# Performance work log

Hardware: AMD Instinct MI355X
Metric: run time of the kernel (lower is better)

Reference implementation:

```python
import jax, jax.numpy as jnp
from jax import lax
import numpy as np

N, T, D_OBS, D_Z, D_U = 32, 1024, 128, 64, 8
H_ENC, H_BW, H_DYN = 256, 128, 256
D_A = 2 * D_Z  # natural-parameter dim (mean-part, precision-part)


def setup_inputs() -> dict:
    key = jax.random.key(0)
    ks = jax.random.split(key, 16)

    def w(k, shape):
        return (jax.random.normal(k, shape, jnp.float32) / np.sqrt(shape[0]).astype(np.float32))

    return {
        "t": jnp.broadcast_to(jnp.arange(T, dtype=jnp.int32), (N, T)),
        "y": jax.random.normal(ks[0], (N, T, D_OBS), jnp.float32),
        "u": 0.1 * jax.random.normal(ks[1], (N, T, D_U), jnp.float32),
        "enc_w1": w(ks[2], (D_OBS, H_ENC)),
        "enc_b1": jnp.zeros((H_ENC,), jnp.float32),
        "enc_w2": w(ks[3], (H_ENC, D_A)),
        "enc_b2": jnp.zeros((D_A,), jnp.float32),
        "bw_wa": w(ks[4], (D_A, H_BW)),
        "bw_wh": w(ks[5], (H_BW, H_BW)),
        "bw_b": jnp.zeros((H_BW,), jnp.float32),
        "bw_wo": w(ks[6], (H_BW, D_A)),
        "bw_bo": jnp.zeros((D_A,), jnp.float32),
        "dyn_w1": w(ks[7], (D_Z + D_U, H_DYN)),
        "dyn_b1": jnp.zeros((H_DYN,), jnp.float32),
        "dyn_w2": w(ks[8], (H_DYN, D_Z)),
        "dyn_b2": jnp.zeros((D_Z,), jnp.float32),
        "q_raw": 0.1 * jax.random.normal(ks[9], (D_Z,), jnp.float32),
        "m0": jnp.zeros((D_Z,), jnp.float32),
        "v0": jnp.ones((D_Z,), jnp.float32),
    }


def _constrain_natural(nat):
    # DiagMVN: first half is the mean-natural-param, second half must be <= 0
    e1, e2 = nat[..., :D_Z], nat[..., D_Z:]
    return jnp.concatenate([e1, -jax.nn.softplus(e2)], axis=-1)


def reference(t, y, u, enc_w1, enc_b1, enc_w2, enc_b2,
              bw_wa, bw_wh, bw_b, bw_wo, bw_bo,
              dyn_w1, dyn_b1, dyn_w2, dyn_b2, q_raw, m0, v0):
    # --- local obs encoder (per-step MLP), dropout prob = 0.0 so mask == 1 ---
    h = jnp.tanh(jnp.einsum('ntd,dh->nth', y, enc_w1) + enc_b1)
    a = jnp.einsum('nth,ha->nta', h, enc_w2) + enc_b2          # [N,T,2Dz]

    # --- backward encoder: reverse recurrence over time (pseudo mode) ---
    a_t = jnp.swapaxes(a, 0, 1)                                # [T,N,2Dz]

    def bw_step(h_next, a_step):
        hcell = jnp.tanh(a_step @ bw_wa + h_next @ bw_wh + bw_b)
        return hcell, hcell @ bw_wo + bw_bo

    _, b_t = lax.scan(bw_step, jnp.zeros((N, H_BW), a.dtype), a_t, reverse=True)
    alpha = _constrain_natural(b_t)                            # [T,N,2Dz]

    # --- vmap'd sequential natural-parameter filter over time ---
    Q = jax.nn.softplus(q_raw)                                 # diag state noise
    u_t = jnp.swapaxes(u, 0, 1)                                # [T,N,Du]

    def step(carry, xs):
        m, v = carry
        alpha_step, u_step = xs
        x = jnp.concatenate([m, u_step], axis=-1)
        m_p = jnp.tanh(x @ dyn_w1 + dyn_b1) @ dyn_w2 + dyn_b2  # predictive mean
        v_p = v + Q                                            # predictive var
        e1 = m_p / v_p + alpha_step[..., :D_Z]
        e2 = -0.5 / v_p + alpha_step[..., D_Z:]                # stays < 0
        v_s = -0.5 / e2
        m_s = v_s * e1
        return (m_s, v_s), (jnp.concatenate([m_s, v_s], -1),
                            jnp.concatenate([m_p, v_p], -1))

    m_init = jnp.broadcast_to(m0, (N, D_Z))
    v_init = jnp.broadcast_to(v0, (N, D_Z))
    _, (moment_s, moment_p) = lax.scan(step, (m_init, v_init), (alpha, u_t))

    out = jnp.concatenate([moment_s, moment_p], axis=-1)       # [T,N,4Dz]
    return jnp.swapaxes(out, 0, 1)                             # [N,T,4Dz]
```

## Files before the change

kernel.cpp:

```cpp
#include <hip/hip_runtime.h>
#include <math.h>

#define T_LEN 1024
#define NB 32

typedef _Float16 h2 __attribute__((ext_vector_type(2)));

__device__ __forceinline__ h2 f2h2(float f) { return __builtin_bit_cast(h2, f); }

__device__ __forceinline__ float dot2(h2 a, h2 b, float c) {
#if __has_builtin(__builtin_amdgcn_fdot2)
    return __builtin_amdgcn_fdot2(a, b, c, false);
#else
    return fmaf((float)a[0], (float)b[0], fmaf((float)a[1], (float)b[1], c));
#endif
}

#define DPP_ADD(v, ctrl) do { \
    int _xi = __builtin_bit_cast(int, v); \
    int _yi = __builtin_amdgcn_update_dpp(_xi, _xi, (ctrl), 0xF, 0xF, true); \
    v += __builtin_bit_cast(float, _yi); } while (0)

__device__ __forceinline__ float softplus_f(float x) {
    return fmaxf(x, 0.f) + log1pf(expf(-fabsf(x)));
}

__device__ __forceinline__ float fast_tanh(float x) {
    float e = __builtin_amdgcn_exp2f(x * 2.88539008177792681472f);
    float r = __builtin_amdgcn_rcpf(1.f + e);
    return 1.f - 2.f * r;
}

__device__ __forceinline__ void bar_sync() {
    asm volatile("s_waitcnt lgkmcnt(0)" ::: "memory");
    __builtin_amdgcn_s_barrier();
    asm volatile("" ::: "memory");
}

__global__ __launch_bounds__(256) void k_encoder(
    const float* __restrict__ y, const float* __restrict__ u,
    const float* __restrict__ w1, const float* __restrict__ b1,
    const float* __restrict__ w2, const float* __restrict__ b2,
    const float* __restrict__ wa, const float* __restrict__ bb,
    const float* __restrict__ dynw1, const float* __restrict__ dynb1,
    float* __restrict__ apre, float* __restrict__ preU)
{
    __shared__ float ly[8][128];
    __shared__ float lh[8][256];
    __shared__ float la[8][128];
    __shared__ float lu[8][8];
    const int tid = threadIdx.x;
    const int row0 = blockIdx.x * 8;

    ((float4*)&ly[0][0])[tid] = ((const float4*)(y + (size_t)row0 * 128))[tid];
    if (tid < 16)
        ((float4*)&lu[0][0])[tid] = ((const float4*)(u + (size_t)row0 * 8))[tid];
    __syncthreads();

    {
        float acc[8] = {0,0,0,0,0,0,0,0};
        for (int i = 0; i < 128; i += 4) {
            float w0 = w1[(i+0)*256 + tid];
            float w1v = w1[(i+1)*256 + tid];
            float w2v = w1[(i+2)*256 + tid];
            float w3 = w1[(i+3)*256 + tid];
            #pragma unroll
            for (int r = 0; r < 8; ++r) {
                float4 yv = *(const float4*)&ly[r][i];
                acc[r] += yv.x*w0 + yv.y*w1v + yv.z*w2v + yv.w*w3;
            }
        }
        float bias = b1[tid];
        #pragma unroll
        for (int r = 0; r < 8; ++r) lh[r][tid] = fast_tanh(acc[r] + bias);
    }
    __syncthreads();

    {
        const int d = tid & 127, rh = tid >> 7;
        float acc[4] = {0,0,0,0};
        for (int i = 0; i < 256; i += 4) {
            float w0 = w2[(i+0)*128 + d];
            float w1v = w2[(i+1)*128 + d];
            float w2v = w2[(i+2)*128 + d];
            float w3 = w2[(i+3)*128 + d];
            #pragma unroll
            for (int q = 0; q < 4; ++q) {
                float4 hv = *(const float4*)&lh[rh*4+q][i];
                acc[q] += hv.x*w0 + hv.y*w1v + hv.z*w2v + hv.w*w3;
            }
        }
        float bias = b2[d];
        #pragma unroll
        for (int q = 0; q < 4; ++q) la[rh*4+q][d] = acc[q] + bias;
    }
    __syncthreads();

    {
        const int j = tid & 127, rh = tid >> 7;
        float acc[4] = {0,0,0,0};
        for (int i = 0; i < 128; i += 4) {
            float w0 = wa[(i+0)*128 + j];
            float w1v = wa[(i+1)*128 + j];
            float w2v = wa[(i+2)*128 + j];
            float w3 = wa[(i+3)*128 + j];
            #pragma unroll
            for (int q = 0; q < 4; ++q) {
                float4 av = *(const float4*)&la[rh*4+q][i];
                acc[q] += av.x*w0 + av.y*w1v + av.z*w2v + av.w*w3;
            }
        }
        float bias = bb[j];
        #pragma unroll
        for (int q = 0; q < 4; ++q) {
            int rn = row0 + rh*4 + q;
            int n = rn >> 10, t = rn & 1023;
            apre[((size_t)t*NB + n)*128 + j] = acc[q] + bias;
        }
    }

    {
        float wu[8];
        #pragma unroll
        for (int c = 0; c < 8; ++c) wu[c] = dynw1[(64 + c)*256 + tid];
        float bias = dynb1[tid];
        #pragma unroll
        for (int r = 0; r < 8; ++r) {
            float acc = bias;
            #pragma unroll
            for (int c = 0; c < 8; ++c) acc += lu[r][c] * wu[c];
            int rn = row0 + r;
            int n = rn >> 10, t = rn & 1023;
            preU[((size_t)t*NB + n)*256 + tid] = acc;
        }
    }
}

__global__ __launch_bounds__(512, 1) void k_bwscan(
    const float* __restrict__ apre, const float* __restrict__ wh,
    float* __restrict__ hcell)
{
    const int n = blockIdx.x;
    const int tid = threadIdx.x;
    const int j = tid >> 2, p = tid & 3;
    __shared__ _Float16 h[2][128];

    h2 w0, w1, w2, w3, w4, w5, w6, w7, w8, w9, w10, w11, w12, w13, w14, w15;
    {
        const float* s = wh + (size_t)(p * 32) * 128 + j;
        w0  = h2{(_Float16)s[0*128],  (_Float16)s[1*128]};
        w1  = h2{(_Float16)s[2*128],  (_Float16)s[3*128]};
        w2  = h2{(_Float16)s[4*128],  (_Float16)s[5*128]};
        w3  = h2{(_Float16)s[6*128],  (_Float16)s[7*128]};
        w4  = h2{(_Float16)s[8*128],  (_Float16)s[9*128]};
        w5  = h2{(_Float16)s[10*128], (_Float16)s[11*128]};
        w6  = h2{(_Float16)s[12*128], (_Float16)s[13*128]};
        w7  = h2{(_Float16)s[14*128], (_Float16)s[15*128]};
        w8  = h2{(_Float16)s[16*128], (_Float16)s[17*128]};
        w9  = h2{(_Float16)s[18*128], (_Float16)s[19*128]};
        w10 = h2{(_Float16)s[20*128], (_Float16)s[21*128]};
        w11 = h2{(_Float16)s[22*128], (_Float16)s[23*128]};
        w12 = h2{(_Float16)s[24*128], (_Float16)s[25*128]};
        w13 = h2{(_Float16)s[26*128], (_Float16)s[27*128]};
        w14 = h2{(_Float16)s[28*128], (_Float16)s[29*128]};
        w15 = h2{(_Float16)s[30*128], (_Float16)s[31*128]};
    }

    if (tid < 128) h[0][tid] = (_Float16)0.f;
    __syncthreads();

    float apA = apre[((size_t)1023*NB + n)*128 + j];
    float apB = apre[((size_t)1022*NB + n)*128 + j];

#define BWSTEP(cur, nxt, apv, tt) do { \
        const _Float16* hb = &h[cur][p*32]; \
        float4 r0 = *(const float4*)hb; \
        float4 r1 = *(const float4*)(hb + 8); \
        float4 r2 = *(const float4*)(hb + 16); \
        float4 r3 = *(const float4*)(hb + 24); \
        float c0 = dot2(f2h2(r0.x), w0, 0.f); \
        float c1 = dot2(f2h2(r0.y), w1, 0.f); \
        float c2 = dot2(f2h2(r0.z), w2, 0.f); \
        float c3 = dot2(f2h2(r0.w), w3, 0.f); \
        c0 = dot2(f2h2(r1.x), w4, c0); \
        c1 = dot2(f2h2(r1.y), w5, c1); \
        c2 = dot2(f2h2(r1.z), w6, c2); \
        c3 = dot2(f2h2(r1.w), w7, c3); \
        c0 = dot2(f2h2(r2.x), w8, c0); \
        c1 = dot2(f2h2(r2.y), w9, c1); \
        c2 = dot2(f2h2(r2.z), w10, c2); \
        c3 = dot2(f2h2(r2.w), w11, c3); \
        c0 = dot2(f2h2(r3.x), w12, c0); \
        c1 = dot2(f2h2(r3.y), w13, c1); \
        c2 = dot2(f2h2(r3.z), w14, c2); \
        c3 = dot2(f2h2(r3.w), w15, c3); \
        float acc = (c0+c1) + (c2+c3); \
        DPP_ADD(acc, 0xB1); \
        DPP_ADD(acc, 0x4E); \
        float hc = fast_tanh(acc + apv); \
        if (p == 0) h[nxt][j] = (_Float16)hc; \
        else if (p == 1) hcell[((size_t)(tt)*NB + n)*128 + j] = hc; \
        bar_sync(); } while (0)

    for (int t = 1023; t > 0; t -= 2) {
        float apN0 = 0.f, apN1 = 0.f;
        if (t - 2 >= 0) apN0 = apre[((size_t)(t-2)*NB + n)*128 + j];
        BWSTEP(0, 1, apA, t);
        if (t - 3 >= 0) apN1 = apre[((size_t)(t-3)*NB + n)*128 + j];
        BWSTEP(1, 0, apB, t - 1);
        apA = apN0; apB = apN1;
    }
#undef BWSTEP
}

__global__ __launch_bounds__(256) void k_alpha(
    const float* __restrict__ hcell, const float* __restrict__ wo,
    const float* __restrict__ bo, float* __restrict__ alpha)
{
    __shared__ float lhc[8][128];
    const int tid = threadIdx.x;
    const size_t base = (size_t)blockIdx.x * 8 * 128;
    ((float4*)&lhc[0][0])[tid] = ((const float4*)(hcell + base))[tid];
    __syncthreads();

    const int j = tid & 127, rh = tid >> 7;
    float acc[4] = {0,0,0,0};
    for (int i = 0; i < 128; i += 4) {
        float w0 = wo[(i+0)*128 + j];
        float w1v = wo[(i+1)*128 + j];
        float w2v = wo[(i+2)*128 + j];
        float w3 = wo[(i+3)*128 + j];
        #pragma unroll
        for (int q = 0; q < 4; ++q) {
            float4 hv = *(const float4*)&lhc[rh*4+q][i];
            acc[q] += hv.x*w0 + hv.y*w1v + hv.z*w2v + hv.w*w3;
        }
    }
    float bias = bo[j];
    const int dpos = (j & 63) * 2 + (j >> 6);
    #pragma unroll
    for (int q = 0; q < 4; ++q) {
        float b = acc[q] + bias;
        float val = (j < 64) ? b : -softplus_f(b);
        alpha[base + (size_t)(rh*4+q)*128 + dpos] = val;
    }
}

#define LHF(x) ((x) + (((x) >> 4) << 3))

__global__ __launch_bounds__(512, 1) void k_fwscan(
    const float* __restrict__ alpha, const float* __restrict__ preU,
    const float* __restrict__ dynw1, const float* __restrict__ dynw2,
    const float* __restrict__ dynb2, const float* __restrict__ qraw,
    const float* __restrict__ m0, const float* __restrict__ v0,
    float* __restrict__ out)
{
    const int n = blockIdx.x;
    const int tid = threadIdx.x;
    const int hh = tid >> 1, pp = tid & 1;
    const int d2 = tid >> 3, qq = tid & 7;
    __shared__ _Float16 lm[2][64];
    __shared__ _Float16 lhid[384];

    h2 u0, u1, u2, u3, u4, u5, u6, u7, u8, u9, ua, ub, uc, ud, ue, uf;
    {
        const float* s = dynw1 + (size_t)(pp * 32) * 256 + hh;
        u0 = h2{(_Float16)s[0*256],  (_Float16)s[1*256]};
        u1 = h2{(_Float16)s[2*256],  (_Float16)s[3*256]};
        u2 = h2{(_Float16)s[4*256],  (_Float16)s[5*256]};
        u3 = h2{(_Float16)s[6*256],  (_Float16)s[7*256]};
        u4 = h2{(_Float16)s[8*256],  (_Float16)s[9*256]};
        u5 = h2{(_Float16)s[10*256], (_Float16)s[11*256]};
        u6 = h2{(_Float16)s[12*256], (_Float16)s[13*256]};
        u7 = h2{(_Float16)s[14*256], (_Float16)s[15*256]};
        u8 = h2{(_Float16)s[16*256], (_Float16)s[17*256]};
        u9 = h2{(_Float16)s[18*256], (_Float16)s[19*256]};
        ua = h2{(_Float16)s[20*256], (_Float16)s[21*256]};
        ub = h2{(_Float16)s[22*256], (_Float16)s[23*256]};
        uc = h2{(_Float16)s[24*256], (_Float16)s[25*256]};
        ud = h2{(_Float16)s[26*256], (_Float16)s[27*256]};
        ue = h2{(_Float16)s[28*256], (_Float16)s[29*256]};
        uf = h2{(_Float16)s[30*256], (_Float16)s[31*256]};
    }
    h2 v0p, v1p, v2p, v3p, v4p, v5p, v6p, v7p;
    h2 v8p, v9p, vap, vbp, vcp, vdp, vep, vfp;
    {
        const float* s = dynw2 + (size_t)(qq * 32) * 64 + d2;
        v0p = h2{(_Float16)s[0*64],  (_Float16)s[1*64]};
        v1p = h2{(_Float16)s[2*64],  (_Float16)s[3*64]};
        v2p = h2{(_Float16)s[4*64],  (_Float16)s[5*64]};
        v3p = h2{(_Float16)s[6*64],  (_Float16)s[7*64]};
        v4p = h2{(_Float16)s[8*64],  (_Float16)s[9*64]};
        v5p = h2{(_Float16)s[10*64], (_Float16)s[11*64]};
        v6p = h2{(_Float16)s[12*64], (_Float16)s[13*64]};
        v7p = h2{(_Float16)s[14*64], (_Float16)s[15*64]};
        v8p = h2{(_Float16)s[16*64], (_Float16)s[17*64]};
        v9p = h2{(_Float16)s[18*64], (_Float16)s[19*64]};
        vap = h2{(_Float16)s[20*64], (_Float16)s[21*64]};
        vbp = h2{(_Float16)s[22*64], (_Float16)s[23*64]};
        vcp = h2{(_Float16)s[24*64], (_Float16)s[25*64]};
        vdp = h2{(_Float16)s[26*64], (_Float16)s[27*64]};
        vep = h2{(_Float16)s[28*64], (_Float16)s[29*64]};
        vfp = h2{(_Float16)s[30*64], (_Float16)s[31*64]};
    }

    const float Qv  = softplus_f(qraw[d2]);
    const float b2v = dynb2[d2];
    float vreg = v0[d2];
    if (tid < 64) lm[0][tid] = (_Float16)m0[tid];

    float hp0 = preU[(size_t)n * 256 + hh];
    float hp1 = preU[((size_t)NB + n)*256 + hh];
    float2 av0 = *(const float2*)&alpha[(size_t)n * 128 + d2*2];
    float2 av1 = *(const float2*)&alpha[((size_t)NB + n)*128 + d2*2];
    __syncthreads();

    int cur = 0;
    for (int t = 0; t < T_LEN; ++t) {
        float hpN = 0.f;
        float2 avN = make_float2(0.f, 0.f);
        if (t + 2 < T_LEN) {
            hpN = preU[((size_t)(t+2)*NB + n)*256 + hh];
            avN = *(const float2*)&alpha[((size_t)(t+2)*NB + n)*128 + d2*2];
        }

        {
            const _Float16* mb = &lm[cur][pp*32];
            float4 r0 = *(const float4*)mb;
            float4 r1 = *(const float4*)(mb + 8);
            float4 r2 = *(const float4*)(mb + 16);
            float4 r3 = *(const float4*)(mb + 24);
            float c0 = dot2(f2h2(r0.x), u0, 0.f);
            float c1 = dot2(f2h2(r0.y), u1, 0.f);
            float c2 = dot2(f2h2(r0.z), u2, 0.f);
            float c3 = dot2(f2h2(r0.w), u3, 0.f);
            c0 = dot2(f2h2(r1.x), u4, c0);
            c1 = dot2(f2h2(r1.y), u5, c1);
            c2 = dot2(f2h2(r1.z), u6, c2);
            c3 = dot2(f2h2(r1.w), u7, c3);
            c0 = dot2(f2h2(r2.x), u8, c0);
            c1 = dot2(f2h2(r2.y), u9, c1);
            c2 = dot2(f2h2(r2.z), ua, c2);
            c3 = dot2(f2h2(r2.w), ub, c3);
            c0 = dot2(f2h2(r3.x), uc, c0);
            c1 = dot2(f2h2(r3.y), ud, c1);
            c2 = dot2(f2h2(r3.z), ue, c2);
            c3 = dot2(f2h2(r3.w), uf, c3);
            float acc = (c0+c1) + (c2+c3);
            DPP_ADD(acc, 0xB1);
            if (pp == 0) lhid[LHF(hh)] = (_Float16)fast_tanh(hp0 + acc);
        }
        bar_sync();

        {
            const _Float16* hbA = &lhid[LHF(qq*32)];
            const _Float16* hbB = &lhid[LHF(qq*32 + 16)];
            float4 r0 = *(const float4*)hbA;
            float4 r1 = *(const float4*)(hbA + 8);
            float4 r2 = *(const float4*)hbB;
            float4 r3 = *(const float4*)(hbB + 8);
            float c0 = dot2(f2h2(r0.x), v0p, 0.f);
            float c1 = dot2(f2h2(r0.y), v1p, 0.f);
            float c2 = dot2(f2h2(r0.z), v2p, 0.f);
            float c3 = dot2(f2h2(r0.w), v3p, 0.f);
            c0 = dot2(f2h2(r1.x), v4p, c0);
            c1 = dot2(f2h2(r1.y), v5p, c1);
            c2 = dot2(f2h2(r1.z), v6p, c2);
            c3 = dot2(f2h2(r1.w), v7p, c3);
            c0 = dot2(f2h2(r2.x), v8p, c0);
            c1 = dot2(f2h2(r2.y), v9p, c1);
            c2 = dot2(f2h2(r2.z), vap, c2);
            c3 = dot2(f2h2(r2.w), vbp, c3);
            c0 = dot2(f2h2(r3.x), vcp, c0);
            c1 = dot2(f2h2(r3.y), vdp, c1);
            c2 = dot2(f2h2(r3.z), vep, c2);
            c3 = dot2(f2h2(r3.w), vfp, c3);
            float acc = (c0+c1) + (c2+c3);
            DPP_ADD(acc, 0xB1);
            DPP_ADD(acc, 0x4E);
            DPP_ADD(acc, 0x141);

            float m_p = acc + b2v;
            float v_p = vreg + Qv;
            float rvp = __builtin_amdgcn_rcpf(v_p);
            float e1 = m_p * rvp + av0.x;
            float e2 = av0.y - 0.5f * rvp;
            float v_s = -0.5f * __builtin_amdgcn_rcpf(e2);
            float m_s = v_s * e1;
            vreg = v_s;
            if (qq == 0) lm[cur ^ 1][d2] = (_Float16)m_s;

            if (qq < 4) {
                size_t ob = ((size_t)n * T_LEN + t) * 256;
                float val = (qq == 0) ? m_s : (qq == 1) ? v_s : (qq == 2) ? m_p : v_p;
                out[ob + (size_t)qq*64 + d2] = val;
            }
        }
        bar_sync();
        cur ^= 1;
        hp0 = hp1; hp1 = hpN;
        av0 = av1; av1 = avN;
    }
}

extern "C" void kernel_launch(void* const* d_in, const int* in_sizes, int n_in,
                              void* d_out, int out_size, void* d_ws, size_t ws_size,
                              hipStream_t stream) {
    const float* y      = (const float*)d_in[1];
    const float* u      = (const float*)d_in[2];
    const float* enc_w1 = (const float*)d_in[3];
    const float* enc_b1 = (const float*)d_in[4];
    const float* enc_w2 = (const float*)d_in[5];
    const float* enc_b2 = (const float*)d_in[6];
    const float* bw_wa  = (const float*)d_in[7];
    const float* bw_wh  = (const float*)d_in[8];
    const float* bw_b   = (const float*)d_in[9];
    const float* bw_wo  = (const float*)d_in[10];
    const float* bw_bo  = (const float*)d_in[11];
    const float* dyn_w1 = (const float*)d_in[12];
    const float* dyn_b1 = (const float*)d_in[13];
    const float* dyn_w2 = (const float*)d_in[14];
    const float* dyn_b2 = (const float*)d_in[15];
    const float* q_raw  = (const float*)d_in[16];
    const float* m0     = (const float*)d_in[17];
    const float* v0     = (const float*)d_in[18];
    float* out = (float*)d_out;

    float* ws = (float*)d_ws;
    float* apre  = ws;
    float* hcell = ws + 4194304;
    float* alpha = ws;
    float* preU  = ws + 2 * 4194304;

    k_encoder<<<4096, 256, 0, stream>>>(y, u, enc_w1, enc_b1, enc_w2, enc_b2,
                                        bw_wa, bw_b, dyn_w1, dyn_b1, apre, preU);
    k_bwscan<<<NB, 512, 0, stream>>>(apre, bw_wh, hcell);
    k_alpha<<<4096, 256, 0, stream>>>(hcell, bw_wo, bw_bo, alpha);
    k_fwscan<<<NB, 512, 0, stream>>>(alpha, preU, dyn_w1, dyn_w2, dyn_b2,
                                     q_raw, m0, v0, out);
}
```

Before: 1.143 ms.

## Halve backward-scan block to 256 threads with two lanes per hidden unit

The backward recurrence kernel now uses 256 threads per sequence, with each hidden unit split across 2 lanes instead of 4. Each lane keeps 64 fp16 weights in registers and reads 64 hidden values per step, so one DPP reduction stage is dropped. Fewer wavefronts take part in each per-step barrier, which should cut sync cost on this latency-bound serial loop. In exchange each lane does twice the dot-product work per step and uses more registers.

```diff
diff --git a/kernel.cpp b/kernel.cpp
--- a/kernel.cpp
+++ b/kernel.cpp
@@ -136,34 +136,21 @@
     }
 }
 
-__global__ __launch_bounds__(512, 1) void k_bwscan(
+__global__ __launch_bounds__(256, 1) void k_bwscan(
     const float* __restrict__ apre, const float* __restrict__ wh,
     float* __restrict__ hcell)
 {
     const int n = blockIdx.x;
     const int tid = threadIdx.x;
-    const int j = tid >> 2, p = tid & 3;
+    const int j = tid >> 1, p = tid & 1;
     __shared__ _Float16 h[2][128];
 
-    h2 w0, w1, w2, w3, w4, w5, w6, w7, w8, w9, w10, w11, w12, w13, w14, w15;
-    {
-        const float* s = wh + (size_t)(p * 32) * 128 + j;
-        w0  = h2{(_Float16)s[0*128],  (_Float16)s[1*128]};
-        w1  = h2{(_Float16)s[2*128],  (_Float16)s[3*128]};
-        w2  = h2{(_Float16)s[4*128],  (_Float16)s[5*128]};
-        w3  = h2{(_Float16)s[6*128],  (_Float16)s[7*128]};
-        w4  = h2{(_Float16)s[8*128],  (_Float16)s[9*128]};
-        w5  = h2{(_Float16)s[10*128], (_Float16)s[11*128]};
-        w6  = h2{(_Float16)s[12*128], (_Float16)s[13*128]};
-        w7  = h2{(_Float16)s[14*128], (_Float16)s[15*128]};
-        w8  = h2{(_Float16)s[16*128], (_Float16)s[17*128]};
-        w9  = h2{(_Float16)s[18*128], (_Float16)s[19*128]};
-        w10 = h2{(_Float16)s[20*128], (_Float16)s[21*128]};
-        w11 = h2{(_Float16)s[22*128], (_Float16)s[23*128]};
-        w12 = h2{(_Float16)s[24*128], (_Float16)s[25*128]};
-        w13 = h2{(_Float16)s[26*128], (_Float16)s[27*128]};
-        w14 = h2{(_Float16)s[28*128], (_Float16)s[29*128]};
-        w15 = h2{(_Float16)s[30*128], (_Float16)s[31*128]};
+    h2 w[32];
+    {
+        const float* s = wh + (size_t)(p * 64) * 128 + j;
+        #pragma unroll
+        for (int k = 0; k < 32; ++k)
+            w[k] = h2{(_Float16)s[(2*k)*128], (_Float16)s[(2*k+1)*128]};
     }
 
     if (tid < 128) h[0][tid] = (_Float16)0.f;
@@ -173,33 +160,23 @@
     float apB = apre[((size_t)1022*NB + n)*128 + j];
 
 #define BWSTEP(cur, nxt, apv, tt) do { \
-        const _Float16* hb = &h[cur][p*32]; \
-        float4 r0 = *(const float4*)hb; \
-        float4 r1 = *(const float4*)(hb + 8); \
-        float4 r2 = *(const float4*)(hb + 16); \
-        float4 r3 = *(const float4*)(hb + 24); \
-        float c0 = dot2(f2h2(r0.x), w0, 0.f); \
-        float c1 = dot2(f2h2(r0.y), w1, 0.f); \
-        float c2 = dot2(f2h2(r0.z), w2, 0.f); \
-        float c3 = dot2(f2h2(r0.w), w3, 0.f); \
-        c0 = dot2(f2h2(r1.x), w4, c0); \
-        c1 = dot2(f2h2(r1.y), w5, c1); \
-        c2 = dot2(f2h2(r1.z), w6, c2); \
-        c3 = dot2(f2h2(r1.w), w7, c3); \
-        c0 = dot2(f2h2(r2.x), w8, c0); \
-        c1 = dot2(f2h2(r2.y), w9, c1); \
-        c2 = dot2(f2h2(r2.z), w10, c2); \
-        c3 = dot2(f2h2(r2.w), w11, c3); \
-        c0 = dot2(f2h2(r3.x), w12, c0); \
-        c1 = dot2(f2h2(r3.y), w13, c1); \
-        c2 = dot2(f2h2(r3.z), w14, c2); \
-        c3 = dot2(f2h2(r3.w), w15, c3); \
+        const _Float16* hb = &h[cur][p*64]; \
+        float4 mr[8]; \
+        _Pragma("unroll") \
+        for (int k = 0; k < 8; ++k) mr[k] = ((const float4*)hb)[k]; \
+        float c0 = 0.f, c1 = 0.f, c2 = 0.f, c3 = 0.f; \
+        _Pragma("unroll") \
+        for (int k = 0; k < 8; ++k) { \
+            c0 = dot2(f2h2(mr[k].x), w[4*k+0], c0); \
+            c1 = dot2(f2h2(mr[k].y), w[4*k+1], c1); \
+            c2 = dot2(f2h2(mr[k].z), w[4*k+2], c2); \
+            c3 = dot2(f2h2(mr[k].w), w[4*k+3], c3); \
+        } \
         float acc = (c0+c1) + (c2+c3); \
         DPP_ADD(acc, 0xB1); \
-        DPP_ADD(acc, 0x4E); \
         float hc = fast_tanh(acc + apv); \
         if (p == 0) h[nxt][j] = (_Float16)hc; \
-        else if (p == 1) hcell[((size_t)(tt)*NB + n)*128 + j] = hc; \
+        else        hcell[((size_t)(tt)*NB + n)*128 + j] = hc; \
         bar_sync(); } while (0)
 
     for (int t = 1023; t > 0; t -= 2) {
@@ -434,7 +411,7 @@
 
     k_encoder<<<4096, 256, 0, stream>>>(y, u, enc_w1, enc_b1, enc_w2, enc_b2,
                                         bw_wa, bw_b, dyn_w1, dyn_b1, apre, preU);
-    k_bwscan<<<NB, 512, 0, stream>>>(apre, bw_wh, hcell);
+    k_bwscan<<<NB, 256, 0, stream>>>(apre, bw_wh, hcell);
     k_alpha<<<4096, 256, 0, stream>>>(hcell, bw_wo, bw_bo, alpha);
     k_fwscan<<<NB, 512, 0, stream>>>(alpha, preU, dyn_w1, dyn_w2, dyn_b2,
                                      q_raw, m0, v0, out);
```

Result: faster. 1.109 ms (-3.0%).
